# Kernel tuning notes

Measured on AMD Instinct MI355X. Metric: run time of the kernel, lower is better.

Reference implementation:

```python
import jax, jax.numpy as jnp
import numpy as np
from jax import lax

B, T = 8192, 2048
INIT_ALPHA = 0.1


def setup_inputs() -> dict:
    key = jax.random.key(0)
    kx, = jax.random.split(key, 1)
    # intermittent demand: small non-negative integers, many exact zeros
    x = jax.random.randint(kx, (B, T), 0, 3).astype(jnp.float32)
    alpha = jnp.full((1, 1), INIT_ALPHA, dtype=jnp.float32)  # learned smoothing weight
    Z0 = jnp.ones((B,), dtype=jnp.float32)  # demand-size state
    V0 = jnp.ones((B,), dtype=jnp.float32)  # inter-demand-interval state
    q0 = jnp.ones((B,), dtype=jnp.float32)  # periods since last nonzero demand
    return {"x": x, "alpha": alpha, "Z0": Z0, "V0": V0, "q0": q0}


def reference(x, alpha, Z0, V0, q0):
    """Croston's method recurrence (sba=False): out_t = Z_t / V_t.

    x: (B, T) demand series; states are per-series scalars carried through a scan.
    """
    a = alpha[0, 0]

    def step(carry, xt):  # xt: (B,)
        Z, V, q = carry
        Z_next = a * xt + (1.0 - a) * Z
        V_next = a * q + (1.0 - a) * V
        nz = xt != 0.0
        Z_next = jnp.where(nz, Z_next, Z)
        V_next = jnp.where(nz, V_next, V)
        q_next = jnp.where(nz, 1.0, q + 1.0)
        out = Z_next / V_next  # sba=False branch
        return (Z_next, V_next, q_next), out

    _, outs = lax.scan(step, (Z0, V0, q0), x.T)  # outs: (T, B)
    return outs.T  # (B, T)
```

## Files before the change

kernel.cpp:

```cpp
#include <hip/hip_runtime.h>
#include <stdint.h>


#define TLEN 2048

typedef float vf4 __attribute__((ext_vector_type(4)));

__global__ __launch_bounds__(256) void croston_kernel(
    const float* __restrict__ x,
    const float* __restrict__ alpha,
    const float* __restrict__ Z0,
    const float* __restrict__ V0,
    const float* __restrict__ q0,
    float* __restrict__ out)
{
    __shared__ __attribute__((aligned(16))) float lds[4][2048];

    const int warp = threadIdx.x >> 6;
    const int lane = threadIdx.x & 63;
    const int wave = blockIdx.x * 4 + warp;
    const int wid0 = wave * 4;
    float* W = lds[warp];

    const float a  = alpha[0];
    const float ma = 1.0f - a;

    const int rg   = lane >> 3;
    const int e    = (lane & 7) ^ rg;
    const int goff = rg * 32 + (e << 2);
    const int l7   = lane & 7;
    const int lbase = lane * 32;

    float zs[4], vs[4], qsx[4];
#pragma unroll
    for (int i = 0; i < 4; ++i) {
        zs[i]  = Z0[wid0 + i];
        vs[i]  = V0[wid0 + i];
        qsx[i] = q0[wid0 + i];
    }

    vf4 buf[2][8];
#pragma unroll
    for (int j = 0; j < 8; ++j)
        buf[0][j] = *(const vf4*)(x + (size_t)wid0 * TLEN + j * 256 + lane * 4);

#pragma unroll
    for (int i = 0; i < 4; ++i) {
        const int wid = wid0 + i;

        if (i < 3) {
#pragma unroll
            for (int j = 0; j < 8; ++j)
                buf[(i + 1) & 1][j] =
                    *(const vf4*)(x + (size_t)(wid + 1) * TLEN + j * 256 + lane * 4);
        }

#pragma unroll
        for (int j = 0; j < 8; ++j)
            *(vf4*)(W + j * 256 + goff) = buf[i & 1][j];
        vf4 xv[8];
#pragma unroll
        for (int m = 0; m < 8; ++m)
            xv[m] = *(const vf4*)(W + lbase + ((m ^ l7) << 2));

        float az = 1.f, bz = 0.f, r = 0.f, s = 0.f, f = 1.f, g = 0.f;
#pragma unroll
        for (int m = 0; m < 8; ++m) {
#pragma unroll
            for (int k = 0; k < 4; ++k) {
                const float xt = xv[m][k];
                const bool  nz = (xt != 0.f);
                const float az_n = ma * az;
                const float bz_n = fmaf(ma, bz, a * xt);
                const float r_n  = fmaf(ma, r, a * f);
                const float s_n  = fmaf(ma, s, a * g);
                az = nz ? az_n : az;
                bz = nz ? bz_n : bz;
                r  = nz ? r_n  : r;
                s  = nz ? s_n  : s;
                g  = nz ? 1.f  : (g + 1.f);
                f  = nz ? 0.f  : f;
            }
        }

#pragma unroll
        for (int d = 1; d < 64; d <<= 1) {
            const float az_o = __shfl_up(az, d);
            const float bz_o = __shfl_up(bz, d);
            const float r_o  = __shfl_up(r,  d);
            const float s_o  = __shfl_up(s,  d);
            const float f_o  = __shfl_up(f,  d);
            const float g_o  = __shfl_up(g,  d);
            if (lane >= d) {
                bz = fmaf(az, bz_o, bz);
                s  = fmaf(az, s_o, fmaf(r, g_o, s));
                r  = fmaf(az, r_o, r * f_o);
                az = az * az_o;
                g  = fmaf(f, g_o, g);
                f  = f * f_o;
            }
        }

        float azE = __shfl_up(az, 1), bzE = __shfl_up(bz, 1);
        float rE  = __shfl_up(r, 1),  sE  = __shfl_up(s, 1);
        float fE  = __shfl_up(f, 1),  gE  = __shfl_up(g, 1);
        if (lane == 0) {
            azE = 1.f; bzE = 0.f; rE = 0.f; sE = 0.f; fE = 1.f; gE = 0.f;
        }

        float Z = fmaf(azE, zs[i], bzE);
        float V = fmaf(azE, vs[i], fmaf(rE, qsx[i], sE));
        float q = fmaf(fE, qsx[i], gE);

#pragma unroll
        for (int m = 0; m < 8; ++m) {
#pragma unroll
            for (int k = 0; k < 4; ++k) {
                const float xt = xv[m][k];
                const bool  nz = (xt != 0.f);
                const float Zn = fmaf(ma, Z, a * xt);
                const float Vn = fmaf(ma, V, a * q);
                Z = nz ? Zn : Z;
                V = nz ? Vn : V;
                q = nz ? 1.f : (q + 1.f);
                xv[m][k] = Z * __builtin_amdgcn_rcpf(V);
            }
        }

#pragma unroll
        for (int m = 0; m < 8; ++m)
            *(vf4*)(W + lbase + ((m ^ l7) << 2)) = xv[m];
#pragma unroll
        for (int j = 0; j < 8; ++j) {
            const vf4 o = *(const vf4*)(W + j * 256 + goff);
            *(vf4*)(out + (size_t)wid * TLEN + j * 256 + lane * 4) = o;
        }
    }
}

extern "C" void kernel_launch(void* const* d_in, const int* in_sizes, int n_in,
                              void* d_out, int out_size, void* d_ws, size_t ws_size,
                              hipStream_t stream) {
    const float* x     = (const float*)d_in[0];
    const float* alpha = (const float*)d_in[1];
    const float* Z0    = (const float*)d_in[2];
    const float* V0    = (const float*)d_in[3];
    const float* q0    = (const float*)d_in[4];
    float* out = (float*)d_out;

    dim3 block(256);
    dim3 grid(512);
    croston_kernel<<<grid, block, 0, stream>>>(x, alpha, Z0, V0, q0, out);
}
```

Baseline: 119.8 us.

## Process two series per wave with packed float2 math and branchless selects

Each wave now handles two series at once instead of four in sequence. The two series are interleaved in vf2 vectors so the compiler can emit packed FP32 instructions. The nz selects are replaced by arithmetic masks built from min(x,1), which assumes inputs are non-negative integers. The grid doubles to 1024 blocks, raising parallelism and removing the serial loop over series, at the cost of more live registers and losing the double-buffered prefetch.

```diff
diff --git a/kernel.cpp b/kernel.cpp
--- a/kernel.cpp
+++ b/kernel.cpp
@@ -5,6 +5,7 @@
 #define TLEN 2048
 
 typedef float vf4 __attribute__((ext_vector_type(4)));
+typedef float vf2 __attribute__((ext_vector_type(2)));
 
 __global__ __launch_bounds__(256) void croston_kernel(
     const float* __restrict__ x,
@@ -19,11 +20,11 @@
     const int warp = threadIdx.x >> 6;
     const int lane = threadIdx.x & 63;
     const int wave = blockIdx.x * 4 + warp;
-    const int wid0 = wave * 4;
+    const int widA = wave * 2;
+    const int widB = widA + 1;
     float* W = lds[warp];
 
-    const float a  = alpha[0];
-    const float ma = 1.0f - a;
+    const float a = alpha[0];
 
     const int rg   = lane >> 3;
     const int e    = (lane & 7) ^ rg;
@@ -31,110 +32,115 @@
     const int l7   = lane & 7;
     const int lbase = lane * 32;
 
-    float zs[4], vs[4], qsx[4];
+    vf4 ldA[8], ldB[8];
 #pragma unroll
-    for (int i = 0; i < 4; ++i) {
-        zs[i]  = Z0[wid0 + i];
-        vs[i]  = V0[wid0 + i];
-        qsx[i] = q0[wid0 + i];
+    for (int j = 0; j < 8; ++j)
+        ldA[j] = *(const vf4*)(x + (size_t)widA * TLEN + j * 256 + lane * 4);
+#pragma unroll
+    for (int j = 0; j < 8; ++j)
+        ldB[j] = *(const vf4*)(x + (size_t)widB * TLEN + j * 256 + lane * 4);
+
+    vf2 Zv = {Z0[widA], Z0[widB]};
+    vf2 Vv = {V0[widA], V0[widB]};
+    vf2 qv = {q0[widA], q0[widB]};
+
+#pragma unroll
+    for (int j = 0; j < 8; ++j) *(vf4*)(W + j * 256 + goff) = ldA[j];
+    vf4 xvA[8];
+#pragma unroll
+    for (int m = 0; m < 8; ++m) xvA[m] = *(const vf4*)(W + lbase + ((m ^ l7) << 2));
+#pragma unroll
+    for (int j = 0; j < 8; ++j) *(vf4*)(W + j * 256 + goff) = ldB[j];
+    vf4 xvB[8];
+#pragma unroll
+    for (int m = 0; m < 8; ++m) xvB[m] = *(const vf4*)(W + lbase + ((m ^ l7) << 2));
+
+    const vf2 v1 = {1.f, 1.f};
+    const vf2 v0 = {0.f, 0.f};
+
+    vf2 az = v1, bz = v0, rr = v0, ss = v0, ff = v1, gg = v0;
+#pragma unroll
+    for (int m = 0; m < 8; ++m) {
+#pragma unroll
+        for (int k = 0; k < 4; ++k) {
+            const vf2 xt = {xvA[m][k], xvB[m][k]};
+            const vf2 z  = v1 - __builtin_elementwise_min(xt, v1);
+            const vf2 wa = a - z * a;
+            const vf2 mm = v1 - wa;
+            const vf2 axt = a * xt;
+            az = mm * az;
+            bz = mm * bz + axt;
+            rr = mm * rr + wa * ff;
+            ss = mm * ss + wa * gg;
+            ff = z * ff;
+            gg = z * gg + v1;
+        }
     }
 
-    vf4 buf[2][8];
 #pragma unroll
-    for (int j = 0; j < 8; ++j)
-        buf[0][j] = *(const vf4*)(x + (size_t)wid0 * TLEN + j * 256 + lane * 4);
+    for (int d = 1; d < 64; d <<= 1) {
+        vf2 az_o, bz_o, r_o, s_o, f_o, g_o;
+        az_o.x = __shfl_up(az.x, d); az_o.y = __shfl_up(az.y, d);
+        bz_o.x = __shfl_up(bz.x, d); bz_o.y = __shfl_up(bz.y, d);
+        r_o.x  = __shfl_up(rr.x, d); r_o.y  = __shfl_up(rr.y, d);
+        s_o.x  = __shfl_up(ss.x, d); s_o.y  = __shfl_up(ss.y, d);
+        f_o.x  = __shfl_up(ff.x, d); f_o.y  = __shfl_up(ff.y, d);
+        g_o.x  = __shfl_up(gg.x, d); g_o.y  = __shfl_up(gg.y, d);
+        if (lane >= d) {
+            bz = az * bz_o + bz;
+            ss = az * s_o + (rr * g_o + ss);
+            rr = az * r_o + rr * f_o;
+            az = az * az_o;
+            gg = ff * g_o + gg;
+            ff = ff * f_o;
+        }
+    }
+
+    vf2 azE, bzE, rE, sE, fE, gE;
+    azE.x = __shfl_up(az.x, 1); azE.y = __shfl_up(az.y, 1);
+    bzE.x = __shfl_up(bz.x, 1); bzE.y = __shfl_up(bz.y, 1);
+    rE.x  = __shfl_up(rr.x, 1); rE.y  = __shfl_up(rr.y, 1);
+    sE.x  = __shfl_up(ss.x, 1); sE.y  = __shfl_up(ss.y, 1);
+    fE.x  = __shfl_up(ff.x, 1); fE.y  = __shfl_up(ff.y, 1);
+    gE.x  = __shfl_up(gg.x, 1); gE.y  = __shfl_up(gg.y, 1);
+    if (lane == 0) {
+        azE = v1; bzE = v0; rE = v0; sE = v0; fE = v1; gE = v0;
+    }
+
+    vf2 Zc = azE * Zv + bzE;
+    vf2 Vc = azE * Vv + (rE * qv + sE);
+    vf2 qc = fE * qv + gE;
 
 #pragma unroll
-    for (int i = 0; i < 4; ++i) {
-        const int wid = wid0 + i;
-
-        if (i < 3) {
+    for (int m = 0; m < 8; ++m) {
 #pragma unroll
-            for (int j = 0; j < 8; ++j)
-                buf[(i + 1) & 1][j] =
-                    *(const vf4*)(x + (size_t)(wid + 1) * TLEN + j * 256 + lane * 4);
+        for (int k = 0; k < 4; ++k) {
+            const vf2 xt = {xvA[m][k], xvB[m][k]};
+            const vf2 z  = v1 - __builtin_elementwise_min(xt, v1);
+            const vf2 wa = a - z * a;
+            const vf2 mm = v1 - wa;
+            const vf2 axt = a * xt;
+            Zc = mm * Zc + axt;
+            Vc = mm * Vc + wa * qc;
+            qc = z * qc + v1;
+            xvA[m][k] = Zc.x * __builtin_amdgcn_rcpf(Vc.x);
+            xvB[m][k] = Zc.y * __builtin_amdgcn_rcpf(Vc.y);
         }
+    }
 
 #pragma unroll
-        for (int j = 0; j < 8; ++j)
-            *(vf4*)(W + j * 256 + goff) = buf[i & 1][j];
-        vf4 xv[8];
+    for (int m = 0; m < 8; ++m) *(vf4*)(W + lbase + ((m ^ l7) << 2)) = xvA[m];
 #pragma unroll
-        for (int m = 0; m < 8; ++m)
-            xv[m] = *(const vf4*)(W + lbase + ((m ^ l7) << 2));
-
-        float az = 1.f, bz = 0.f, r = 0.f, s = 0.f, f = 1.f, g = 0.f;
+    for (int j = 0; j < 8; ++j) {
+        const vf4 o = *(const vf4*)(W + j * 256 + goff);
+        *(vf4*)(out + (size_t)widA * TLEN + j * 256 + lane * 4) = o;
+    }
 #pragma unroll
-        for (int m = 0; m < 8; ++m) {
+    for (int m = 0; m < 8; ++m) *(vf4*)(W + lbase + ((m ^ l7) << 2)) = xvB[m];
 #pragma unroll
-            for (int k = 0; k < 4; ++k) {
-                const float xt = xv[m][k];
-                const bool  nz = (xt != 0.f);
-                const float az_n = ma * az;
-                const float bz_n = fmaf(ma, bz, a * xt);
-                const float r_n  = fmaf(ma, r, a * f);
-                const float s_n  = fmaf(ma, s, a * g);
-                az = nz ? az_n : az;
-                bz = nz ? bz_n : bz;
-                r  = nz ? r_n  : r;
-                s  = nz ? s_n  : s;
-                g  = nz ? 1.f  : (g + 1.f);
-                f  = nz ? 0.f  : f;
-            }
-        }
-
-#pragma unroll
-        for (int d = 1; d < 64; d <<= 1) {
-            const float az_o = __shfl_up(az, d);
-            const float bz_o = __shfl_up(bz, d);
-            const float r_o  = __shfl_up(r,  d);
-            const float s_o  = __shfl_up(s,  d);
-            const float f_o  = __shfl_up(f,  d);
-            const float g_o  = __shfl_up(g,  d);
-            if (lane >= d) {
-                bz = fmaf(az, bz_o, bz);
-                s  = fmaf(az, s_o, fmaf(r, g_o, s));
-                r  = fmaf(az, r_o, r * f_o);
-                az = az * az_o;
-                g  = fmaf(f, g_o, g);
-                f  = f * f_o;
-            }
-        }
-
-        float azE = __shfl_up(az, 1), bzE = __shfl_up(bz, 1);
-        float rE  = __shfl_up(r, 1),  sE  = __shfl_up(s, 1);
-        float fE  = __shfl_up(f, 1),  gE  = __shfl_up(g, 1);
-        if (lane == 0) {
-            azE = 1.f; bzE = 0.f; rE = 0.f; sE = 0.f; fE = 1.f; gE = 0.f;
-        }
-
-        float Z = fmaf(azE, zs[i], bzE);
-        float V = fmaf(azE, vs[i], fmaf(rE, qsx[i], sE));
-        float q = fmaf(fE, qsx[i], gE);
-
-#pragma unroll
-        for (int m = 0; m < 8; ++m) {
-#pragma unroll
-            for (int k = 0; k < 4; ++k) {
-                const float xt = xv[m][k];
-                const bool  nz = (xt != 0.f);
-                const float Zn = fmaf(ma, Z, a * xt);
-                const float Vn = fmaf(ma, V, a * q);
-                Z = nz ? Zn : Z;
-                V = nz ? Vn : V;
-                q = nz ? 1.f : (q + 1.f);
-                xv[m][k] = Z * __builtin_amdgcn_rcpf(V);
-            }
-        }
-
-#pragma unroll
-        for (int m = 0; m < 8; ++m)
-            *(vf4*)(W + lbase + ((m ^ l7) << 2)) = xv[m];
-#pragma unroll
-        for (int j = 0; j < 8; ++j) {
-            const vf4 o = *(const vf4*)(W + j * 256 + goff);
-            *(vf4*)(out + (size_t)wid * TLEN + j * 256 + lane * 4) = o;
-        }
+    for (int j = 0; j < 8; ++j) {
+        const vf4 o = *(const vf4*)(W + j * 256 + goff);
+        *(vf4*)(out + (size_t)widB * TLEN + j * 256 + lane * 4) = o;
     }
 }
 
@@ -149,6 +155,6 @@
     float* out = (float*)d_out;
 
     dim3 block(256);
-    dim3 grid(512);
+    dim3 grid(1024);
     croston_kernel<<<grid, block, 0, stream>>>(x, alpha, Z0, V0, q0, out);
 }
```

Measured after the change: 127.9 us. 6.8% more time.
